# Kernel tuning notes

Hardware: AMD Instinct MI355X
Metric: run time of the kernel (lower is better)

## Reference

```python
import jax, jax.numpy as jnp
import numpy as np

N = 100_000   # nodes (batched over G graphs)
E = 3_200_000 # edges (avg degree 32)
G = 64        # graphs in the batch
IN_FEATS, H1, H3, NUM_CLASSES = 64, 64, 64, 2


def setup_inputs() -> dict:
    key = jax.random.key(0)
    ks = jax.random.split(key, 11)
    return {
        "in_feat": jax.random.normal(ks[0], (N, IN_FEATS), jnp.float32),
        "edge_weights": jax.random.uniform(ks[1], (E,), jnp.float32, 1e-3, 1.0),
        "W1": jax.random.normal(ks[2], (IN_FEATS, H1), jnp.float32) / np.sqrt(IN_FEATS),
        "b1": jnp.zeros((H1,), jnp.float32),
        "W2": jax.random.normal(ks[3], (H1, H3), jnp.float32) / np.sqrt(H1),
        "b2": jnp.zeros((H3,), jnp.float32),
        "Wc": jax.random.normal(ks[4], (H3, NUM_CLASSES), jnp.float32) / np.sqrt(H3),
        "bc": jnp.zeros((NUM_CLASSES,), jnp.float32),
        "edge_src": jax.random.randint(ks[5], (E,), 0, N, jnp.int32),
        "edge_dst": jax.random.randint(ks[6], (E,), 0, N, jnp.int32),
        "graph_ids": jnp.sort(jax.random.randint(ks[7], (N,), 0, G, jnp.int32)),
    }


def reference(in_feat, edge_weights, W1, b1, W2, b2, Wc, bc,
              edge_src, edge_dst, graph_ids):
    # EdgeWeightNorm(norm='right'): w_e / (sum of weights into dst(e))
    deg_w = jax.ops.segment_sum(edge_weights, edge_dst, num_segments=N)  # [N]
    nw = edge_weights / deg_w[edge_dst]                                  # [E]

    # unweighted in-degree used by SAGEConv 'gcn' aggregator
    deg = jax.ops.segment_sum(jnp.ones((E,), jnp.float32), edge_dst, num_segments=N)  # [N]

    def sage_gcn(h, W, b):
        # weighted neighbor sum: sum_e nw_e * h[src_e] scattered to dst
        msg = h[edge_src] * nw[:, None]                                  # [E, F]
        neigh = jax.ops.segment_sum(msg, edge_dst, num_segments=N)      # [N, F]
        h_neigh = (neigh + h) / (deg[:, None] + 1.0)                     # gcn: include self, /(deg+1)
        return h_neigh @ W + b                                           # fc_neigh + bias

    h = jax.nn.relu(sage_gcn(in_feat, W1, b1))
    h = jax.nn.relu(sage_gcn(h, W2, b2))

    # dgl.mean_nodes: per-graph mean of node features
    counts = jax.ops.segment_sum(jnp.ones((N,), jnp.float32), graph_ids, num_segments=G)
    hg = jax.ops.segment_sum(h, graph_ids, num_segments=G) / jnp.maximum(counts, 1.0)[:, None]

    return hg @ Wc + bc  # [G, num_classes]
```

## Files before the change

kernel.cpp:

```cpp
#include <hip/hip_runtime.h>
#include <hip/hip_fp16.h>


#define BK   1024
#define NB   128
#define CAPB 5120
#define CAPP 6144
#define SRC17 0x1FFFFu

__device__ __forceinline__ float readlane_f(float v, int l) {
    return __int_as_float(__builtin_amdgcn_readlane(__float_as_int(v), l));
}

__device__ __forceinline__ int2 ntload_i2(const int2* p) {
    unsigned long long r = __builtin_nontemporal_load((const unsigned long long*)p);
    return make_int2((int)(unsigned)(r & 0xffffffffull), (int)(unsigned)(r >> 32));
}

__global__ void k_cvt(const float4* __restrict__ x, uint2* __restrict__ xh, int n4) {
    int i = blockIdx.x * blockDim.x + threadIdx.x;
    if (i >= n4) return;
    float4 v = x[i];
    __half2 a = __floats2half2_rn(v.x, v.y);
    __half2 b = __floats2half2_rn(v.z, v.w);
    uint2 r;
    r.x = *(const unsigned*)&a;
    r.y = *(const unsigned*)&b;
    xh[i] = r;
}

__global__ __launch_bounds__(1024) void k_binB(
        const int* __restrict__ esrc, const int* __restrict__ edst,
        const float* __restrict__ ew, int* __restrict__ cursor,
        int2* __restrict__ bsw, int E, int CH) {
    __shared__ int h[BK];
    __shared__ int lcur[BK];
    const int tid = threadIdx.x;

    if (tid < BK) h[tid] = 0;
    __syncthreads();
    const int e0 = blockIdx.x * CH;
    const int e1 = min(E, e0 + CH);
    for (int e = e0 + tid; e < e1; e += 1024)
        atomicAdd(&h[edst[e] >> 7], 1);
    __syncthreads();
    if (tid < BK) {
        int c = h[tid];
        lcur[tid] = c ? atomicAdd(&cursor[tid], c) : 0;
    }
    __syncthreads();
    for (int e = e0 + tid; e < e1; e += 1024) {
        int d = edst[e];
        int b = d >> 7;
        int p = atomicAdd(&lcur[b], 1);
        if (p < CAPB)
            bsw[(size_t)b * CAPB + p] =
                make_int2(((d & 127) << 18) | esrc[e], __float_as_int(ew[e]));
    }
}

__global__ __launch_bounds__(512) void k_csrsort(
        const int2* __restrict__ bsw, const int* __restrict__ cursor,
        unsigned* __restrict__ csr, int* __restrict__ off, int* __restrict__ fill,
        int N) {
    __shared__ unsigned se[CAPP];
    __shared__ int cur[NB];
    __shared__ int pfx[NB];
    __shared__ int tot;
    const int b = blockIdx.x, tid = threadIdx.x;
    for (int i = tid; i < CAPP; i += 512) se[i] = 0u;
    if (tid < NB) cur[tid] = 0;
    __syncthreads();
    const int cnt = min(cursor[b], CAPB);
    const int2* __restrict__ eb = bsw + (size_t)b * CAPB;
    for (int i = tid; i < cnt; i += 512)
        atomicAdd(&cur[eb[i].x >> 18], 1);
    __syncthreads();
    int pc = 0;
    if (tid < NB) {
        int c0 = cur[tid & ~1], c1 = cur[tid | 1];
        pc = (max(c0, c1) + 7) & ~7;
        pfx[tid] = pc;
    }
    __syncthreads();
    for (int o = 1; o < NB; o <<= 1) {
        int t = 0;
        if (tid < NB && tid >= o) t = pfx[tid - o];
        __syncthreads();
        if (tid < NB) pfx[tid] += t;
        __syncthreads();
    }
    if (tid < NB) {
        int excl = pfx[tid] - pc;
        int node = b * NB + tid;
        if (node < N) { off[node] = b * CAPP + excl; fill[node] = cur[tid]; }
        cur[tid] = excl;
        if (tid == NB - 1) tot = min(pfx[tid], CAPP);
    }
    __syncthreads();
    for (int i = tid; i < cnt; i += 512) {
        int2 e = eb[i];
        int p = atomicAdd(&cur[e.x >> 18], 1);
        unsigned h15 = (unsigned)__half_as_ushort(
                           __float2half_rn(__int_as_float(e.y))) & 0x7FFFu;
        if (p < CAPP)
            se[p] = ((unsigned)e.x & SRC17) | (h15 << 17);
    }
    __syncthreads();
    const int T = tot;
    unsigned* __restrict__ cb = csr + (size_t)b * CAPP;
    for (int i = tid; i < T; i += 512) cb[i] = se[i];
}

__global__ void k_fill_pad(const int* __restrict__ esrc, const int* __restrict__ edst,
                           const float* __restrict__ ew, int* __restrict__ fill,
                           int2* __restrict__ csr, int E, int CAP) {
    int e = blockIdx.x * blockDim.x + threadIdx.x;
    if (e < E) {
        int d = edst[e];
        int p = atomicAdd(&fill[d], 1);
        if (p < CAP)
            csr[(size_t)d * CAP + p] = make_int2(esrc[e], __float_as_int(ew[e]));
    }
}

__global__ void k_cnt(const int* __restrict__ edst, int* __restrict__ cnt, int E) {
    int e = blockIdx.x * blockDim.x + threadIdx.x;
    if (e < E) atomicAdd(&cnt[edst[e]], 1);
}

__global__ void k_off(const int* __restrict__ cnt, int* __restrict__ off,
                      int* __restrict__ fill, int* __restrict__ cursor, int N) {
    int i    = blockIdx.x * blockDim.x + threadIdx.x;
    int lane = threadIdx.x & 63;
    int c    = (i < N) ? cnt[i] : 0;
    int pref = c;
    #pragma unroll
    for (int d = 1; d < 64; d <<= 1) {
        int t = __shfl_up(pref, d);
        if (lane >= d) pref += t;
    }
    int total = __shfl(pref, 63);
    int base  = 0;
    if (lane == 63) base = atomicAdd(cursor, total);
    base = __shfl(base, 63);
    if (i < N) {
        int p = base + pref - c;
        off[i]  = p;
        fill[i] = p;
    }
}

__global__ void k_fill(const int* __restrict__ esrc, const int* __restrict__ edst,
                       const float* __restrict__ ew, int* __restrict__ fill,
                       int2* __restrict__ csr, int E) {
    int e = blockIdx.x * blockDim.x + threadIdx.x;
    if (e < E) {
        int d = edst[e];
        int p = atomicAdd(&fill[d], 1);
        csr[p] = make_int2(esrc[e], __float_as_int(ew[e]));
    }
}

__global__ __launch_bounds__(256, 6) void k_agg_p(
        const unsigned* __restrict__ xh, const int* __restrict__ off,
        const int* __restrict__ cnt_arr, const unsigned* __restrict__ csr,
        unsigned* __restrict__ aggh, int N) {
    const int lane = threadIdx.x & 63;
    const int slot = lane >> 5;
    const int f8   = lane & 31;
    const int wq   = (blockIdx.x * blockDim.x + threadIdx.x) >> 6;
    const int nw   = (gridDim.x * blockDim.x) >> 6;
    const int npair = (N + 1) >> 1;

    for (int pr = wq; pr < npair; pr += nw) {
        const int  node  = 2 * pr + slot;
        const bool valid = node < N;
        const int  cnt_s = valid ? cnt_arr[node] : 0;
        const int  st_s  = valid ? off[node] : 0;
        const int  cA = __builtin_amdgcn_readlane(cnt_s, 0);
        const int  cB = __builtin_amdgcn_readlane(cnt_s, 32);
        const int  pc = (max(cA, cB) + 7) & ~7;

        float2 acc = {0.f, 0.f};
        float  sw  = 0.f;
        const unsigned* __restrict__ pS = csr + st_s;
        for (int k = 0; k < pc; k += 8) {
            uint4 e0 = *(const uint4*)(pS + k);
            uint4 e1 = *(const uint4*)(pS + k + 4);
            unsigned ev[8] = {e0.x, e0.y, e0.z, e0.w, e1.x, e1.y, e1.z, e1.w};
            float    w[8];
            unsigned u[8];
            #pragma unroll
            for (int t = 0; t < 8; ++t) {
                unsigned e = ev[t];
                w[t] = __half2float(__ushort_as_half((unsigned short)(e >> 17)));
                u[t] = xh[((e & SRC17) << 5) | (unsigned)f8];
            }
            #pragma unroll
            for (int t = 0; t < 8; ++t) {
                float2 v = __half22float2(*(const __half2*)&u[t]);
                acc.x = fmaf(w[t], v.x, acc.x);
                acc.y = fmaf(w[t], v.y, acc.y);
                sw += w[t];
            }
        }
        if (valid) {
            float invw = (sw > 0.f) ? (1.f / sw) : 0.f;
            float invd = 1.f / ((float)cnt_s + 1.f);
            unsigned us = xh[((unsigned)node << 5) | (unsigned)f8];
            float2 xs = __half22float2(*(const __half2*)&us);
            float hx = (acc.x * invw + xs.x) * invd;
            float hy = (acc.y * invw + xs.y) * invd;
            __half2 hp = __floats2half2_rn(hx, hy);
            __builtin_nontemporal_store(*(const unsigned*)&hp,
                                        &aggh[(size_t)node * 32 + f8]);
        }
    }
}

__global__ __launch_bounds__(256, 4) void k_agg_f(
        const unsigned* __restrict__ xh, const int* __restrict__ off,
        const int* __restrict__ cnt_arr, const int2* __restrict__ csr,
        unsigned* __restrict__ aggh, int N, int CAP) {
    const int lane   = threadIdx.x & 63;
    const int slot   = lane >> 5;
    const int f8     = lane & 31;
    const int wave   = (blockIdx.x * blockDim.x + threadIdx.x) >> 6;
    const int nwaves = (gridDim.x * blockDim.x) >> 6;

    int node  = wave;
    int cnt_p = 0, start_p = 0;
    if (node < N) {
        cnt_p   = cnt_arr[node];
        start_p = (CAP > 0) ? node * CAP : off[node];
        if (CAP > 0) cnt_p = min(cnt_p, CAP);
    }
    for (; node < N; node += nwaves) {
        const int cnt = cnt_p, start = start_p;
        int nn = node + nwaves;
        if (nn < N) {
            cnt_p   = cnt_arr[nn];
            start_p = (CAP > 0) ? nn * CAP : off[nn];
            if (CAP > 0) cnt_p = min(cnt_p, CAP);
        }
        int2 ee = make_int2(0, 0);
        if (lane < cnt) ee = ntload_i2(&csr[start + lane]);
        float2 acc0 = {0.f, 0.f}, acc1 = {0.f, 0.f};
        float  sw = 0.0f;
        for (int bk = 0; bk < cnt; bk += 64) {
            int   s_l = ee.x;
            float w_l = __int_as_float(ee.y);
            int2 en = make_int2(0, 0);
            int  rem = cnt - bk - 64;
            if (lane < rem) en = ntload_i2(&csr[start + bk + 64 + lane]);
            sw += w_l;
            #pragma unroll
            for (int half = 0; half < 2; ++half) {
                float    w[16];
                unsigned u[16];
                #pragma unroll
                for (int k = 0; k < 16; ++k) {
                    int idx = half * 32 + 2 * k + slot;
                    int s   = __shfl(s_l, idx);
                    w[k]    = __shfl(w_l, idx);
                    u[k]    = xh[(size_t)s * 32 + f8];
                }
                #pragma unroll
                for (int k = 0; k < 16; k += 2) {
                    float2 v0 = __half22float2(*(const __half2*)&u[k]);
                    float2 v1 = __half22float2(*(const __half2*)&u[k + 1]);
                    acc0.x = fmaf(w[k],     v0.x, acc0.x);
                    acc0.y = fmaf(w[k],     v0.y, acc0.y);
                    acc1.x = fmaf(w[k + 1], v1.x, acc1.x);
                    acc1.y = fmaf(w[k + 1], v1.y, acc1.y);
                }
            }
            ee = en;
        }
        acc0.x += acc1.x; acc0.y += acc1.y;
        acc0.x += __shfl_xor(acc0.x, 32);
        acc0.y += __shfl_xor(acc0.y, 32);
        #pragma unroll
        for (int mask = 1; mask <= 32; mask <<= 1) sw += __shfl_xor(sw, mask);
        float invw = (sw > 0.0f) ? (1.0f / sw) : 0.0f;
        float invd = 1.0f / ((float)cnt + 1.0f);
        if (lane < 32) {
            unsigned us = xh[(size_t)node * 32 + f8];
            float2 xs = __half22float2(*(const __half2*)&us);
            float hx = (acc0.x * invw + xs.x) * invd;
            float hy = (acc0.y * invw + xs.y) * invd;
            __half2 hp = __floats2half2_rn(hx, hy);
            __builtin_nontemporal_store(*(const unsigned*)&hp,
                                        &aggh[(size_t)node * 32 + f8]);
        }
    }
}

__global__ __launch_bounds__(256) void k_fc(
        const __half* __restrict__ agg, const float* __restrict__ W,
        const float* __restrict__ b, __half* __restrict__ outh, int N) {
    const int lane   = threadIdx.x & 63;
    const int wave   = (blockIdx.x * blockDim.x + threadIdx.x) >> 6;
    const int nwaves = (gridDim.x * blockDim.x) >> 6;
    float wc[64];
    #pragma unroll
    for (int f = 0; f < 64; ++f) wc[f] = W[f * 64 + lane];
    const float bias = b[lane];
    for (int node = wave; node < N; node += nwaves) {
        float hn = __half2float(agg[(size_t)node * 64 + lane]);
        float o0 = bias, o1 = 0.f, o2 = 0.f, o3 = 0.f;
        #pragma unroll
        for (int f = 0; f < 64; f += 4) {
            o0 = fmaf(readlane_f(hn, f),     wc[f],     o0);
            o1 = fmaf(readlane_f(hn, f + 1), wc[f + 1], o1);
            o2 = fmaf(readlane_f(hn, f + 2), wc[f + 2], o2);
            o3 = fmaf(readlane_f(hn, f + 3), wc[f + 3], o3);
        }
        float o = fmaxf((o0 + o1) + (o2 + o3), 0.0f);
        outh[(size_t)node * 64 + lane] = __float2half_rn(o);
    }
}

__global__ __launch_bounds__(256) void k_fcpool(
        const __half* __restrict__ agg, const float* __restrict__ W,
        const float* __restrict__ b, const int* __restrict__ gid,
        float* __restrict__ hg, float* __restrict__ cntg, int N) {
    const int lane   = threadIdx.x & 63;
    const int wave   = (blockIdx.x * blockDim.x + threadIdx.x) >> 6;
    const int nwaves = (gridDim.x * blockDim.x) >> 6;
    float wc[64];
    #pragma unroll
    for (int f = 0; f < 64; ++f) wc[f] = W[f * 64 + lane];
    const float bias = b[lane];
    const int per   = (N + nwaves - 1) / nwaves;
    const int start = wave * per;
    const int end   = min(N, start + per);
    if (start >= N) return;

    int   curg = -1;
    float acc  = 0.0f;
    int   c    = 0;
    for (int node = start; node < end; ++node) {
        float hn = __half2float(agg[(size_t)node * 64 + lane]);
        float o0 = bias, o1 = 0.f, o2 = 0.f, o3 = 0.f;
        #pragma unroll
        for (int f = 0; f < 64; f += 4) {
            o0 = fmaf(readlane_f(hn, f),     wc[f],     o0);
            o1 = fmaf(readlane_f(hn, f + 1), wc[f + 1], o1);
            o2 = fmaf(readlane_f(hn, f + 2), wc[f + 2], o2);
            o3 = fmaf(readlane_f(hn, f + 3), wc[f + 3], o3);
        }
        float o = fmaxf((o0 + o1) + (o2 + o3), 0.0f);
        int g = gid[node];
        if (g != curg) {
            if (c > 0) {
                atomicAdd(&hg[curg * 64 + lane], acc);
                if (lane == 0) atomicAdd(&cntg[curg], (float)c);
            }
            curg = g; acc = 0.0f; c = 0;
        }
        acc += o;
        ++c;
    }
    if (c > 0) {
        atomicAdd(&hg[curg * 64 + lane], acc);
        if (lane == 0) atomicAdd(&cntg[curg], (float)c);
    }
}

__global__ void k_out(const float* __restrict__ hg, const float* __restrict__ cntg,
                      const float* __restrict__ Wc, const float* __restrict__ bc,
                      float* __restrict__ out, int G) {
    int t = blockIdx.x * blockDim.x + threadIdx.x;
    if (t >= G * 2) return;
    int g = t >> 1, c = t & 1;
    float ct = fmaxf(cntg[g], 1.0f);
    float o  = bc[c];
    for (int f = 0; f < 64; ++f)
        o += (hg[g * 64 + f] / ct) * Wc[f * 2 + c];
    out[t] = o;
}

extern "C" void kernel_launch(void* const* d_in, const int* in_sizes, int n_in,
                              void* d_out, int out_size, void* d_ws, size_t ws_size,
                              hipStream_t stream) {
    const float* in_feat = (const float*)d_in[0];
    const float* ew      = (const float*)d_in[1];
    const float* W1      = (const float*)d_in[2];
    const float* b1      = (const float*)d_in[3];
    const float* W2      = (const float*)d_in[4];
    const float* b2      = (const float*)d_in[5];
    const float* Wc      = (const float*)d_in[6];
    const float* bc      = (const float*)d_in[7];
    const int*   esrc    = (const int*)d_in[8];
    const int*   edst    = (const int*)d_in[9];
    const int*   gid     = (const int*)d_in[10];

    const int E = in_sizes[1];
    const int N = in_sizes[10];
    const int G = out_size / 2;
    float* outp = (float*)d_out;

    auto alignup = [](size_t x) { return (x + 15) & ~(size_t)15; };
    char* base = (char*)d_ws;
    const int FC_BLK = 1024, AGG_BLK = 2048;
    const int n4 = N * 16;

    const int B   = (N + NB - 1) / NB;
    const int CHB = (E + 255) / 256;

    size_t zhdr  = ((size_t)G * 64 + G + BK) * 4;
    size_t o_off = alignup(zhdr);
    size_t o_fil = o_off + alignup((size_t)N * 4);
    size_t o_bsw = o_fil + alignup((size_t)N * 4);
    size_t o_csr = o_bsw + alignup((size_t)B * CAPB * 8);
    size_t o_t1  = o_csr + alignup((size_t)B * CAPP * 4);
    size_t o_t2  = o_t1 + alignup((size_t)N * 64 * 2);
    size_t o_xh  = o_t2 + alignup((size_t)N * 64 * 2);
    size_t o_th  = o_xh + alignup((size_t)N * 64 * 2);
    size_t needB = o_th + (size_t)N * 64 * 2;

    bool cap_ok = ((size_t)E / B) + 512 < CAPB && N <= (1 << 17);

    if (ws_size >= needB && B <= BK && cap_ok) {
        float*    hg     = (float*)base;
        float*    cntg   = hg + (size_t)G * 64;
        int*      cursor = (int*)(cntg + G);
        int*      off    = (int*)(base + o_off);
        int*      fill   = (int*)(base + o_fil);
        int2*     bsw    = (int2*)(base + o_bsw);
        unsigned* csr    = (unsigned*)(base + o_csr);
        unsigned* t1h    = (unsigned*)(base + o_t1);
        unsigned* t2h    = (unsigned*)(base + o_t2);
        unsigned* xh0    = (unsigned*)(base + o_xh);
        __half*   th1    = (__half*)(base + o_th);

        hipMemsetAsync(d_ws, 0, zhdr, stream);
        k_cvt    <<<(n4 + 255) / 256, 256, 0, stream>>>((const float4*)in_feat, (uint2*)xh0, n4);
        k_binB   <<<256, 1024, 0, stream>>>(esrc, edst, ew, cursor, bsw, E, CHB);
        k_csrsort<<<B, 512, 0, stream>>>(bsw, cursor, csr, off, fill, N);
        k_agg_p <<<AGG_BLK, 256, 0, stream>>>(xh0, off, fill, csr, t1h, N);
        k_fc    <<<FC_BLK, 256, 0, stream>>>((const __half*)t1h, W1, b1, th1, N);
        k_agg_p <<<AGG_BLK, 256, 0, stream>>>((const unsigned*)th1, off, fill, csr, t2h, N);
        k_fcpool<<<FC_BLK, 256, 0, stream>>>((const __half*)t2h, W2, b2, gid, hg, cntg, N);
        k_out   <<<1, 128, 0, stream>>>(hg, cntg, Wc, bc, outp, G);
        return;
    }

    const int CAP = 96;
    size_t hdr    = ((size_t)G * 64 + G + 1 + N) * 4;
    size_t needB2 = alignup(hdr) + alignup((size_t)N * CAP * 8)
                  + alignup((size_t)N * 64 * 2) * 4;
    if (ws_size >= needB2) {
        size_t o = 0;
        float* hg     = (float*)(base + o);
        float* cntg   = hg + (size_t)G * 64;
        int*   fill   = (int*)(cntg + G) + 1;
        o += alignup(hdr);
        int2*     csr = (int2*)(base + o);     o += alignup((size_t)N * CAP * 8);
        unsigned* t1h = (unsigned*)(base + o); o += alignup((size_t)N * 64 * 2);
        unsigned* t2h = (unsigned*)(base + o); o += alignup((size_t)N * 64 * 2);
        unsigned* xh0 = (unsigned*)(base + o); o += alignup((size_t)N * 64 * 2);
        __half*   th1 = (__half*)(base + o);

        hipMemsetAsync(d_ws, 0, hdr, stream);
        k_cvt     <<<(n4 + 255) / 256, 256, 0, stream>>>((const float4*)in_feat, (uint2*)xh0, n4);
        k_fill_pad<<<(E + 255) / 256, 256, 0, stream>>>(esrc, edst, ew, fill, csr, E, CAP);
        k_agg_f <<<AGG_BLK, 256, 0, stream>>>(xh0, (const int*)nullptr, fill, csr, t1h, N, CAP);
        k_fc    <<<FC_BLK, 256, 0, stream>>>((const __half*)t1h, W1, b1, th1, N);
        k_agg_f <<<AGG_BLK, 256, 0, stream>>>((const unsigned*)th1, (const int*)nullptr, fill, csr, t2h, N, CAP);
        k_fcpool<<<FC_BLK, 256, 0, stream>>>((const __half*)t2h, W2, b2, gid, hg, cntg, N);
        k_out   <<<1, 128, 0, stream>>>(hg, cntg, Wc, bc, outp, G);
        return;
    }

    {
        size_t o = 0;
        float* hg     = (float*)(base + o);
        float* cntg   = hg + (size_t)G * 64;
        int*   cursor = (int*)(cntg + G);
        int*   cnt    = cursor + 1;
        o += alignup(hdr);
        int*      off  = (int*)(base + o);     o += alignup((size_t)N * 4);
        int*      fill = (int*)(base + o);     o += alignup((size_t)N * 4);
        int2*     csr  = (int2*)(base + o);    o += alignup((size_t)E * 8);
        unsigned* t1h  = (unsigned*)(base + o); o += alignup((size_t)N * 64 * 2);
        unsigned* t2h  = (unsigned*)(base + o); o += alignup((size_t)N * 64 * 2);
        unsigned* xh0  = (unsigned*)(base + o); o += alignup((size_t)N * 64 * 2);
        __half*   th1  = (__half*)(base + o);

        hipMemsetAsync(d_ws, 0, hdr, stream);
        k_cvt <<<(n4 + 255) / 256, 256, 0, stream>>>((const float4*)in_feat, (uint2*)xh0, n4);
        k_cnt <<<(E + 255) / 256, 256, 0, stream>>>(edst, cnt, E);
        k_off <<<(N + 255) / 256, 256, 0, stream>>>(cnt, off, fill, cursor, N);
        k_fill<<<(E + 255) / 256, 256, 0, stream>>>(esrc, edst, ew, fill, csr, E);
        k_agg_f <<<AGG_BLK, 256, 0, stream>>>(xh0, off, cnt, csr, t1h, N, 0);
        k_fc    <<<FC_BLK, 256, 0, stream>>>((const __half*)t1h, W1, b1, th1, N);
        k_agg_f <<<AGG_BLK, 256, 0, stream>>>((const unsigned*)th1, off, cnt, csr, t2h, N, 0);
        k_fcpool<<<FC_BLK, 256, 0, stream>>>((const __half*)t2h, W2, b2, gid, hg, cntg, N);
        k_out   <<<1, 128, 0, stream>>>(hg, cntg, Wc, bc, outp, G);
    }
}
```

Measured before the change: 374.8 us.

## Aggregate directly from dst-binned edges with fixed-point LDS atomics, dropping CSR sort

Removes the per-block CSR sort kernel and the CSR-based aggregation kernel. Each block now walks its dst-bucket of binned edges directly and accumulates weighted neighbor features into shared memory with integer fixed-point atomics, along with weight sums and degrees, then normalizes and writes the output. This saves one kernel launch and the CSR build traffic. The cost is 64 LDS atomics per edge, one block per bucket, and reading 8-byte binned edges instead of 4-byte packed CSR entries. Fixed-point scaling adds quantization error and could overflow for large values.

```diff
diff --git a/kernel.cpp b/kernel.cpp
--- a/kernel.cpp
+++ b/kernel.cpp
@@ -5,8 +5,9 @@
 #define BK   1024
 #define NB   128
 #define CAPB 5120
-#define CAPP 6144
 #define SRC17 0x1FFFFu
+#define SCX  16384.0f
+#define SCW  131072.0f
 
 __device__ __forceinline__ float readlane_f(float v, int l) {
     return __int_as_float(__builtin_amdgcn_readlane(__float_as_int(v), l));
@@ -59,57 +60,63 @@
     }
 }
 
-__global__ __launch_bounds__(512) void k_csrsort(
-        const int2* __restrict__ bsw, const int* __restrict__ cursor,
-        unsigned* __restrict__ csr, int* __restrict__ off, int* __restrict__ fill,
+__global__ __launch_bounds__(512) void k_aggI(
+        const __half* __restrict__ xhh, const int2* __restrict__ bsw,
+        const int* __restrict__ cursor, unsigned short* __restrict__ outh,
         int N) {
-    __shared__ unsigned se[CAPP];
-    __shared__ int cur[NB];
-    __shared__ int pfx[NB];
-    __shared__ int tot;
-    const int b = blockIdx.x, tid = threadIdx.x;
-    for (int i = tid; i < CAPP; i += 512) se[i] = 0u;
-    if (tid < NB) cur[tid] = 0;
+    __shared__ int accI[NB * 64];
+    __shared__ int accW[NB];
+    __shared__ int accD[NB];
+    const int tid  = threadIdx.x;
+    const int b    = blockIdx.x;
+    const int lane = tid & 63;
+    const int wv   = tid >> 6;
+    const int node0 = b * NB;
+
+    for (int i = tid; i < NB * 64; i += 512) accI[i] = 0;
+    if (tid < NB) { accW[tid] = 0; accD[tid] = 0; }
     __syncthreads();
+
     const int cnt = min(cursor[b], CAPB);
     const int2* __restrict__ eb = bsw + (size_t)b * CAPB;
-    for (int i = tid; i < cnt; i += 512)
-        atomicAdd(&cur[eb[i].x >> 18], 1);
+
+    for (int i = wv; i < cnt; i += 32) {
+        int2  ee[4];
+        float vh[4];
+        #pragma unroll
+        for (int t = 0; t < 4; ++t) {
+            int idx = i + t * 8;
+            ee[t] = (idx < cnt) ? eb[idx] : make_int2(0, 0);
+        }
+        #pragma unroll
+        for (int t = 0; t < 4; ++t)
+            vh[t] = __half2float(
+                xhh[((size_t)(unsigned)(ee[t].x & SRC17) << 6) | (unsigned)lane]);
+        #pragma unroll
+        for (int t = 0; t < 4; ++t) {
+            if (i + t * 8 < cnt) {
+                int   dl = ee[t].x >> 18;
+                float w  = __int_as_float(ee[t].y);
+                atomicAdd(&accI[dl * 64 + lane], __float2int_rn(w * vh[t] * SCX));
+                if (lane == 0) atomicAdd(&accW[dl], __float2int_rn(w * SCW));
+                if (lane == 1) atomicAdd(&accD[dl], 1);
+            }
+        }
+    }
     __syncthreads();
-    int pc = 0;
-    if (tid < NB) {
-        int c0 = cur[tid & ~1], c1 = cur[tid | 1];
-        pc = (max(c0, c1) + 7) & ~7;
-        pfx[tid] = pc;
-    }
-    __syncthreads();
-    for (int o = 1; o < NB; o <<= 1) {
-        int t = 0;
-        if (tid < NB && tid >= o) t = pfx[tid - o];
-        __syncthreads();
-        if (tid < NB) pfx[tid] += t;
-        __syncthreads();
-    }
-    if (tid < NB) {
-        int excl = pfx[tid] - pc;
-        int node = b * NB + tid;
-        if (node < N) { off[node] = b * CAPP + excl; fill[node] = cur[tid]; }
-        cur[tid] = excl;
-        if (tid == NB - 1) tot = min(pfx[tid], CAPP);
-    }
-    __syncthreads();
-    for (int i = tid; i < cnt; i += 512) {
-        int2 e = eb[i];
-        int p = atomicAdd(&cur[e.x >> 18], 1);
-        unsigned h15 = (unsigned)__half_as_ushort(
-                           __float2half_rn(__int_as_float(e.y))) & 0x7FFFu;
-        if (p < CAPP)
-            se[p] = ((unsigned)e.x & SRC17) | (h15 << 17);
-    }
-    __syncthreads();
-    const int T = tot;
-    unsigned* __restrict__ cb = csr + (size_t)b * CAPP;
-    for (int i = tid; i < T; i += 512) cb[i] = se[i];
+
+    for (int r = wv; r < NB; r += 8) {
+        int node = node0 + r;
+        if (node >= N) continue;
+        float sw   = (float)accW[r] * (1.f / SCW);
+        float invw = (sw > 0.f) ? (1.f / sw) : 0.f;
+        float invd = 1.f / ((float)accD[r] + 1.f);
+        float xs = __half2float(xhh[((size_t)node << 6) | (unsigned)lane]);
+        float a  = (float)accI[r * 64 + lane] * (1.f / SCX);
+        float v  = (a * invw + xs) * invd;
+        outh[(size_t)node * 64 + lane] =
+            __half_as_ushort(__float2half_rn(v));
+    }
 }
 
 __global__ void k_fill_pad(const int* __restrict__ esrc, const int* __restrict__ edst,
@@ -159,63 +166,6 @@
         int d = edst[e];
         int p = atomicAdd(&fill[d], 1);
         csr[p] = make_int2(esrc[e], __float_as_int(ew[e]));
-    }
-}
-
-__global__ __launch_bounds__(256, 6) void k_agg_p(
-        const unsigned* __restrict__ xh, const int* __restrict__ off,
-        const int* __restrict__ cnt_arr, const unsigned* __restrict__ csr,
-        unsigned* __restrict__ aggh, int N) {
-    const int lane = threadIdx.x & 63;
-    const int slot = lane >> 5;
-    const int f8   = lane & 31;
-    const int wq   = (blockIdx.x * blockDim.x + threadIdx.x) >> 6;
-    const int nw   = (gridDim.x * blockDim.x) >> 6;
-    const int npair = (N + 1) >> 1;
-
-    for (int pr = wq; pr < npair; pr += nw) {
-        const int  node  = 2 * pr + slot;
-        const bool valid = node < N;
-        const int  cnt_s = valid ? cnt_arr[node] : 0;
-        const int  st_s  = valid ? off[node] : 0;
-        const int  cA = __builtin_amdgcn_readlane(cnt_s, 0);
-        const int  cB = __builtin_amdgcn_readlane(cnt_s, 32);
-        const int  pc = (max(cA, cB) + 7) & ~7;
-
-        float2 acc = {0.f, 0.f};
-        float  sw  = 0.f;
-        const unsigned* __restrict__ pS = csr + st_s;
-        for (int k = 0; k < pc; k += 8) {
-            uint4 e0 = *(const uint4*)(pS + k);
-            uint4 e1 = *(const uint4*)(pS + k + 4);
-            unsigned ev[8] = {e0.x, e0.y, e0.z, e0.w, e1.x, e1.y, e1.z, e1.w};
-            float    w[8];
-            unsigned u[8];
-            #pragma unroll
-            for (int t = 0; t < 8; ++t) {
-                unsigned e = ev[t];
-                w[t] = __half2float(__ushort_as_half((unsigned short)(e >> 17)));
-                u[t] = xh[((e & SRC17) << 5) | (unsigned)f8];
-            }
-            #pragma unroll
-            for (int t = 0; t < 8; ++t) {
-                float2 v = __half22float2(*(const __half2*)&u[t]);
-                acc.x = fmaf(w[t], v.x, acc.x);
-                acc.y = fmaf(w[t], v.y, acc.y);
-                sw += w[t];
-            }
-        }
-        if (valid) {
-            float invw = (sw > 0.f) ? (1.f / sw) : 0.f;
-            float invd = 1.f / ((float)cnt_s + 1.f);
-            unsigned us = xh[((unsigned)node << 5) | (unsigned)f8];
-            float2 xs = __half22float2(*(const __half2*)&us);
-            float hx = (acc.x * invw + xs.x) * invd;
-            float hy = (acc.y * invw + xs.y) * invd;
-            __half2 hp = __floats2half2_rn(hx, hy);
-            __builtin_nontemporal_store(*(const unsigned*)&hp,
-                                        &aggh[(size_t)node * 32 + f8]);
-        }
     }
 }
 
@@ -411,11 +361,8 @@
     const int CHB = (E + 255) / 256;
 
     size_t zhdr  = ((size_t)G * 64 + G + BK) * 4;
-    size_t o_off = alignup(zhdr);
-    size_t o_fil = o_off + alignup((size_t)N * 4);
-    size_t o_bsw = o_fil + alignup((size_t)N * 4);
-    size_t o_csr = o_bsw + alignup((size_t)B * CAPB * 8);
-    size_t o_t1  = o_csr + alignup((size_t)B * CAPP * 4);
+    size_t o_bsw = alignup(zhdr);
+    size_t o_t1  = o_bsw + alignup((size_t)B * CAPB * 8);
     size_t o_t2  = o_t1 + alignup((size_t)N * 64 * 2);
     size_t o_xh  = o_t2 + alignup((size_t)N * 64 * 2);
     size_t o_th  = o_xh + alignup((size_t)N * 64 * 2);
@@ -424,27 +371,23 @@
     bool cap_ok = ((size_t)E / B) + 512 < CAPB && N <= (1 << 17);
 
     if (ws_size >= needB && B <= BK && cap_ok) {
-        float*    hg     = (float*)base;
-        float*    cntg   = hg + (size_t)G * 64;
-        int*      cursor = (int*)(cntg + G);
-        int*      off    = (int*)(base + o_off);
-        int*      fill   = (int*)(base + o_fil);
-        int2*     bsw    = (int2*)(base + o_bsw);
-        unsigned* csr    = (unsigned*)(base + o_csr);
-        unsigned* t1h    = (unsigned*)(base + o_t1);
-        unsigned* t2h    = (unsigned*)(base + o_t2);
-        unsigned* xh0    = (unsigned*)(base + o_xh);
-        __half*   th1    = (__half*)(base + o_th);
+        float*          hg     = (float*)base;
+        float*          cntg   = hg + (size_t)G * 64;
+        int*            cursor = (int*)(cntg + G);
+        int2*           bsw    = (int2*)(base + o_bsw);
+        unsigned short* t1h    = (unsigned short*)(base + o_t1);
+        unsigned short* t2h    = (unsigned short*)(base + o_t2);
+        unsigned*       xh0    = (unsigned*)(base + o_xh);
+        __half*         th1    = (__half*)(base + o_th);
 
         hipMemsetAsync(d_ws, 0, zhdr, stream);
-        k_cvt    <<<(n4 + 255) / 256, 256, 0, stream>>>((const float4*)in_feat, (uint2*)xh0, n4);
-        k_binB   <<<256, 1024, 0, stream>>>(esrc, edst, ew, cursor, bsw, E, CHB);
-        k_csrsort<<<B, 512, 0, stream>>>(bsw, cursor, csr, off, fill, N);
-        k_agg_p <<<AGG_BLK, 256, 0, stream>>>(xh0, off, fill, csr, t1h, N);
-        k_fc    <<<FC_BLK, 256, 0, stream>>>((const __half*)t1h, W1, b1, th1, N);
-        k_agg_p <<<AGG_BLK, 256, 0, stream>>>((const unsigned*)th1, off, fill, csr, t2h, N);
+        k_cvt  <<<(n4 + 255) / 256, 256, 0, stream>>>((const float4*)in_feat, (uint2*)xh0, n4);
+        k_binB <<<256, 1024, 0, stream>>>(esrc, edst, ew, cursor, bsw, E, CHB);
+        k_aggI <<<B, 512, 0, stream>>>((const __half*)xh0, bsw, cursor, t1h, N);
+        k_fc   <<<FC_BLK, 256, 0, stream>>>((const __half*)t1h, W1, b1, th1, N);
+        k_aggI <<<B, 512, 0, stream>>>(th1, bsw, cursor, t2h, N);
         k_fcpool<<<FC_BLK, 256, 0, stream>>>((const __half*)t2h, W2, b2, gid, hg, cntg, N);
-        k_out   <<<1, 128, 0, stream>>>(hg, cntg, Wc, bc, outp, G);
+        k_out  <<<1, 128, 0, stream>>>(hg, cntg, Wc, bc, outp, G);
         return;
     }
 
```

Result: slower. 639.0 us (+70.5%).
